# Kernel tuning notes

Measured on AMD Instinct MI355X. Metric: run time of the kernel, lower is better.

The kernel has to match this reference:

```python
import jax, jax.numpy as jnp
import numpy as np

B, PS, E, A, EMB, D, V, LC, TCAP = 128, 14, 2048, 512, 512, 512, 10000, 128, 26
T = TCAP - 1  # max decode length


def setup_inputs() -> dict:
    key = jax.random.key(0)
    ks = jax.random.split(key, 16)
    g = lambda k, shape: jax.random.normal(k, shape, jnp.float32) * 0.02
    cap_len = jax.random.randint(ks[2], (B, 1), 2, TCAP + 1).at[0, 0].set(TCAP)
    return {
        "encoder_out": jax.random.normal(ks[0], (B, PS, PS, E), jnp.float32),
        "encoded_captions": jax.random.randint(ks[1], (B, TCAP), 0, V),
        "caption_lengths": cap_len,
        "length_class": jax.random.randint(ks[3], (B,), 0, 3),
        "W_enc_att": g(ks[4], (E, A)), "b_enc_att": jnp.zeros((A,), jnp.float32),
        "W_dec_att": g(ks[5], (D, A)), "b_dec_att": jnp.zeros((A,), jnp.float32),
        "w_full_att": g(ks[6], (A,)), "b_full_att": jnp.zeros((), jnp.float32),
        "W_init_h": g(ks[7], (E, D)), "b_init_h": jnp.zeros((D,), jnp.float32),
        "W_init_c": g(ks[8], (E, D)), "b_init_c": jnp.zeros((D,), jnp.float32),
        "W_fbeta": g(ks[9], (D, E)), "b_fbeta": jnp.zeros((E,), jnp.float32),
        "emb_table": jax.random.uniform(ks[10], (V, EMB), jnp.float32, -0.1, 0.1),
        "lc_table": jax.random.uniform(ks[11], (3, LC), jnp.float32, -0.1, 0.1),
        "W_fc": jax.random.uniform(ks[12], (D, V), jnp.float32, -0.1, 0.1),
        "b_fc": jnp.zeros((V,), jnp.float32),
        "W_ih": g(ks[13], (EMB + E + LC, 4 * D)), "b_ih": jnp.zeros((4 * D,), jnp.float32),
        "W_hh": g(ks[14], (D, 4 * D)), "b_hh": jnp.zeros((4 * D,), jnp.float32),
    }


def reference(encoder_out, encoded_captions, caption_lengths, length_class,
              W_enc_att, b_enc_att, W_dec_att, b_dec_att, w_full_att, b_full_att,
              W_init_h, b_init_h, W_init_c, b_init_c, W_fbeta, b_fbeta,
              emb_table, lc_table, W_fc, b_fc, W_ih, b_ih, W_hh, b_hh):
    enc = encoder_out.reshape(B, -1, E)                      # [B, P, E]
    cap_len = caption_lengths[:, 0]
    sort_ind = jnp.argsort(-cap_len)                          # descending by length
    enc = enc[sort_ind]
    caps = encoded_captions[sort_ind]
    style = lc_table[length_class[sort_ind]]                  # [B, LC]
    dec_len = cap_len[sort_ind] - 1                           # [B]

    embs = emb_table[caps]                                    # [B, TCAP, EMB]
    mean_enc = enc.mean(axis=1)
    h0 = mean_enc @ W_init_h + b_init_h
    c0 = mean_enc @ W_init_c + b_init_c
    # encoder side of attention is time-invariant: precompute once
    att1 = jnp.einsum('bpe,ea->bpa', enc, W_enc_att) + b_enc_att

    def step(carry, xs):
        h, c = carry
        t, emb_t = xs
        att2 = h @ W_dec_att + b_dec_att
        e = jnp.einsum('bpa,a->bp', jax.nn.relu(att1 + att2[:, None, :]), w_full_att) + b_full_att
        alpha = jax.nn.softmax(e, axis=1)                     # [B, P]
        awe = jnp.einsum('bpe,bp->be', enc, alpha)
        gate = jax.nn.sigmoid(h @ W_fbeta + b_fbeta)
        x = jnp.concatenate([emb_t, style, gate * awe], axis=1)
        gates = x @ W_ih + b_ih + h @ W_hh + b_hh             # [B, 4D], order i,f,g,o
        i, f, g, o = jnp.split(gates, 4, axis=1)
        c_new = jax.nn.sigmoid(f) * c + jax.nn.sigmoid(i) * jnp.tanh(g)
        h_new = jax.nn.sigmoid(o) * jnp.tanh(c_new)
        preds = h_new @ W_fc + b_fc                           # dropout is identity in eval
        m = (t < dec_len)[:, None]                            # active sequences at step t
        return ((jnp.where(m, h_new, h), jnp.where(m, c_new, c)),
                (jnp.where(m, preds, 0.0), jnp.where(m, alpha, 0.0)))

    ts = jnp.arange(T)
    emb_seq = jnp.swapaxes(embs[:, :T, :], 0, 1)              # [T, B, EMB]
    _, (preds, alphas) = jax.lax.scan(step, (h0, c0), (ts, emb_seq))
    predictions = jnp.swapaxes(preds, 0, 1)                   # [B, T, V]
    alphas = jnp.swapaxes(alphas, 0, 1)                       # [B, T, P]
    return predictions, caps, dec_len, alphas, sort_ind
```

## Files before the change

### kernel.cpp

```cpp
#include <hip/hip_runtime.h>
#include <math.h>

constexpr int kB   = 128;
constexpr int kP   = 196;
constexpr int kE   = 2048;
constexpr int kA   = 512;
constexpr int kEMB = 512;
constexpr int kD   = 512;
constexpr int kV   = 10000;
constexpr int kLC  = 128;
constexpr int kTCAP= 26;
constexpr int kT   = 25;
constexpr int kX   = kEMB + kLC + kE;
constexpr int kXH  = kX + kD;
constexpr int kN3  = kV + kA + kE;
constexpr int kBIG = 1 << 30;
constexpr int KZ   = 5;

typedef __attribute__((ext_vector_type(8))) short bf8;
typedef __attribute__((ext_vector_type(4))) float f4;

__device__ inline float b2f(ushort u) { return __uint_as_float(((unsigned)u) << 16); }
__device__ inline ushort f2b(float f) {
    unsigned u = __float_as_uint(f);
    return (ushort)((u + 0x7fffu + ((u >> 16) & 1u)) >> 16);
}

#define SWZ(r, k) ((((r) * 32) + (k)) ^ (((r) & 7) << 3))

__global__ __launch_bounds__(128) void sort_setup(
    const int* __restrict__ caplen, const int* __restrict__ caps_in,
    const int* __restrict__ lclass, const float* __restrict__ lc_table,
    int* __restrict__ sort_ind, int* __restrict__ declen, int* __restrict__ caps_i,
    float* __restrict__ style,
    float* __restrict__ out_caps, float* __restrict__ out_declen,
    float* __restrict__ out_sortind)
{
    __shared__ int lens[kB];
    __shared__ int sind[kB];
    int i = threadIdx.x;
    lens[i] = caplen[i];
    __syncthreads();
    int li = lens[i];
    int r = 0;
    for (int j = 0; j < kB; j++) {
        int lj = lens[j];
        if (lj > li || (lj == li && j < i)) r++;
    }
    sind[r] = i;
    sort_ind[r] = i;
    out_sortind[r] = (float)i;
    __syncthreads();
    int orig = sind[i];
    int dl = lens[orig] - 1;
    declen[i] = dl;
    out_declen[i] = (float)dl;
    for (int t = 0; t < kTCAP; t++) {
        int cv = caps_in[orig * kTCAP + t];
        caps_i[i * kTCAP + t] = cv;
        out_caps[i * kTCAP + t] = (float)cv;
    }
    int lcl = lclass[orig];
    for (int k = 0; k < kLC; k++) style[i * kLC + k] = lc_table[lcl * kLC + k];
}

__global__ __launch_bounds__(256) void tcvt_kernel(
    const float* __restrict__ src, int ldsrc, int K, int N,
    ushort* __restrict__ dst, long long ldd)
{
    __shared__ float tile[32][33];
    int k0 = blockIdx.y * 32, n0 = blockIdx.x * 32;
    int tx = threadIdx.x & 31, ty = threadIdx.x >> 5;
    #pragma unroll
    for (int j = 0; j < 4; j++) {
        int k = k0 + ty + j * 8, n = n0 + tx;
        tile[ty + j * 8][tx] = (k < K && n < N) ? src[(long long)k * ldsrc + n] : 0.f;
    }
    __syncthreads();
    #pragma unroll
    for (int j = 0; j < 4; j++) {
        int n = n0 + ty + j * 8, k = k0 + tx;
        if (n < N && k < K) dst[(long long)n * ldd + k] = f2b(tile[tx][ty + j * 8]);
    }
}

__global__ __launch_bounds__(256) void bias_setup_kernel(
    const float* __restrict__ b_fc, const float* __restrict__ b_dec,
    const float* __restrict__ b_fb, const float* __restrict__ b_ih0,
    const float* __restrict__ b_ic0, const float* __restrict__ b_ih,
    const float* __restrict__ b_hh,
    float* __restrict__ bias3, float* __restrict__ bias_hc, float* __restrict__ gbias)
{
    int idx = blockIdx.x * 256 + threadIdx.x;
    if (idx < kN3) {
        float v;
        if (idx < kV) v = b_fc[idx];
        else if (idx < kV + kA) v = b_dec[idx - kV];
        else v = b_fb[idx - kV - kA];
        bias3[idx] = v;
    } else if (idx < kN3 + 1024) {
        int i = idx - kN3;
        bias_hc[i] = (i < 512) ? b_ih0[i] : b_ic0[i - 512];
    } else if (idx < kN3 + 1024 + 2048) {
        int i = idx - kN3 - 1024;
        gbias[i] = b_ih[i] + b_hh[i];
    }
}

__global__ __launch_bounds__(256) void enc_cvt_kernel(
    const float* __restrict__ enc, const int* __restrict__ sort_ind,
    ushort* __restrict__ enc_bf)
{
    long long idx4 = (long long)blockIdx.x * 256 + threadIdx.x;
    if (idx4 >= (long long)kB * kP * kE / 4) return;
    int r = (int)(idx4 >> 9);
    int cc = ((int)idx4 & 511) * 4;
    int b = r / kP, p = r - b * kP;
    long long srow = (long long)sort_ind[b] * kP + p;
    float4 v = *(const float4*)(enc + srow * kE + cc);
    ushort4 o; o.x = f2b(v.x); o.y = f2b(v.y); o.z = f2b(v.z); o.w = f2b(v.w);
    *(ushort4*)(enc_bf + (long long)r * kE + cc) = o;
}

__global__ __launch_bounds__(256) void mean_enc_kernel(
    const float* __restrict__ encf, const ushort* __restrict__ encb, int use_bf,
    const int* __restrict__ sort_ind, float* __restrict__ me)
{
    int idx = blockIdx.x * 256 + threadIdx.x;
    int b = idx >> 11, e = idx & 2047;
    float s = 0.f;
    if (use_bf) {
        const ushort* base = encb + (long long)b * kP * kE + e;
        #pragma unroll 4
        for (int p = 0; p < kP; p++) s += b2f(base[(long long)p * kE]);
    } else {
        const float* base = encf + (long long)sort_ind[b] * kP * kE + e;
        #pragma unroll 4
        for (int p = 0; p < kP; p++) s += base[(long long)p * kE];
    }
    me[idx] = s * (1.0f / 196.0f);
}

__global__ __launch_bounds__(256) void gemm2(
    const void* __restrict__ Am, int lda, int a_bf16,
    const ushort* __restrict__ Bt, int ldbt,
    const float* __restrict__ bias,
    void* __restrict__ out1, long long ldc1, int c1_bf16,
    int split1, float* __restrict__ out2, long long ldc2,
    int split2, float* __restrict__ out3, long long ldc3,
    const int* __restrict__ declen, int t, int pred_mode,
    int M, int N, int K, long long zstride)
{
    __shared__ short As[64 * 32];
    __shared__ short Bs[128 * 32];
    int tid = threadIdx.x;
    int lane = tid & 63, w = tid >> 6, quad = lane >> 4, l16 = lane & 15;
    int m0 = blockIdx.y * 64, n0 = blockIdx.x * 128;

    f4 acc[8];
    #pragma unroll
    for (int i = 0; i < 8; i++) acc[i] = (f4){0.f, 0.f, 0.f, 0.f};

    int a_r = tid >> 2;
    int a_kc = (tid & 3) * 8;
    long long a_row = m0 + a_r;
    const float*  a_srcf = (const float*)Am  + a_row * (long long)lda + a_kc;
    const ushort* a_srcb = (const ushort*)Am + a_row * (long long)lda + a_kc;

    int b_r = tid >> 1;
    int b_kc = (tid & 1) * 16;
    bool bvalid = (n0 + b_r) < N;
    const ushort* b_src = Bt + (long long)(n0 + b_r) * ldbt + b_kc;

    int kpb = K / (int)gridDim.z;
    int kbeg = (int)blockIdx.z * kpb, kend = kbeg + kpb;

    float4 af0 = make_float4(0.f, 0.f, 0.f, 0.f), af1 = af0;
    uint4 au, bu0, bu1;
    au.x = au.y = au.z = au.w = 0u; bu0 = au; bu1 = au;

    if (a_bf16) au = *(const uint4*)(a_srcb + kbeg);
    else { af0 = *(const float4*)(a_srcf + kbeg); af1 = *(const float4*)(a_srcf + kbeg + 4); }
    if (bvalid) { bu0 = *(const uint4*)(b_src + kbeg); bu1 = *(const uint4*)(b_src + kbeg + 8); }

    for (int k0 = kbeg; k0 < kend; k0 += 32) {
        __syncthreads();
        if (a_bf16) {
            *(uint4*)&As[SWZ(a_r, a_kc)] = au;
        } else {
            uint4 pk; ushort* pp = (ushort*)&pk;
            pp[0] = f2b(af0.x); pp[1] = f2b(af0.y); pp[2] = f2b(af0.z); pp[3] = f2b(af0.w);
            pp[4] = f2b(af1.x); pp[5] = f2b(af1.y); pp[6] = f2b(af1.z); pp[7] = f2b(af1.w);
            *(uint4*)&As[SWZ(a_r, a_kc)] = pk;
        }
        *(uint4*)&Bs[SWZ(b_r, b_kc)]     = bu0;
        *(uint4*)&Bs[SWZ(b_r, b_kc + 8)] = bu1;
        int kn = k0 + 32;
        if (kn < kend) {
            if (a_bf16) au = *(const uint4*)(a_srcb + kn);
            else { af0 = *(const float4*)(a_srcf + kn); af1 = *(const float4*)(a_srcf + kn + 4); }
            if (bvalid) { bu0 = *(const uint4*)(b_src + kn); bu1 = *(const uint4*)(b_src + kn + 8); }
        }
        __syncthreads();
        bf8 a = *(const bf8*)&As[SWZ(w * 16 + l16, quad * 8)];
        #pragma unroll
        for (int nt = 0; nt < 8; nt++) {
            bf8 b = *(const bf8*)&Bs[SWZ(nt * 16 + l16, quad * 8)];
            acc[nt] = __builtin_amdgcn_mfma_f32_16x16x32_bf16(a, b, acc[nt], 0, 0, 0);
        }
    }

    long long zoff = (long long)blockIdx.z * zstride;
    #pragma unroll
    for (int nt = 0; nt < 8; nt++) {
        int cn = n0 + nt * 16 + l16;
        if (cn >= N) continue;
        float bv = bias ? bias[cn] : 0.f;
        #pragma unroll
        for (int reg = 0; reg < 4; reg++) {
            int rr = m0 + w * 16 + quad * 4 + reg;
            float v = acc[nt][reg] + bv;
            if (cn < split1) {
                long long idx;
                if (pred_mode) {
                    int bb = rr & 127, tt = rr >> 7;
                    if (tt >= declen[bb]) v = 0.f;
                    idx = ((long long)bb * kT + tt) * ldc1 + cn;
                } else {
                    if (declen && t >= declen[rr]) v = 0.f;
                    idx = (long long)rr * ldc1 + cn + zoff;
                }
                if (c1_bf16) ((ushort*)out1)[idx] = f2b(v);
                else         ((float*)out1)[idx] = v;
            } else if (cn < split2) {
                out2[(long long)rr * ldc2 + (cn - split1)] = v;
            } else {
                out3[(long long)rr * ldc3 + (cn - split2)] = v;
            }
        }
    }
}

__global__ __launch_bounds__(512) void attn_softmax_kernel(
    const ushort* __restrict__ att1, const float* __restrict__ att2,
    const float* __restrict__ w_full, const float* __restrict__ b_full,
    float* __restrict__ alpha, float* __restrict__ alphas_out,
    const int* __restrict__ declen, int t, const int* __restrict__ smap)
{
    int b = blockIdx.x;
    int ob = smap ? smap[b] : b;
    __shared__ float es[kP];
    __shared__ float red1[8], red2[8];
    int tid = threadIdx.x;
    int wave = tid >> 6, lane = tid & 63;
    float a2r[8], wfr[8];
    {
        const float4* ap = (const float4*)(att2 + (long long)b * kA + lane * 8);
        *(float4*)&a2r[0] = ap[0]; *(float4*)&a2r[4] = ap[1];
        const float4* wp = (const float4*)(w_full + lane * 8);
        *(float4*)&wfr[0] = wp[0]; *(float4*)&wfr[4] = wp[1];
    }
    float bf = b_full[0];
    const ushort* a1base = att1 + (long long)ob * kP * kA + lane * 8;
    for (int p0 = 0; p0 < kP; p0 += 8) {
        int p = p0 + wave;
        if (p < kP) {
            uint4 u = *(const uint4*)(a1base + (long long)p * kA);
            const unsigned* uw = (const unsigned*)&u;
            float s = 0.f;
            #pragma unroll
            for (int j = 0; j < 4; j++) {
                unsigned x = uw[j];
                float v0 = b2f((ushort)(x & 0xffffu)) + a2r[2 * j];
                float v1 = b2f((ushort)(x >> 16))     + a2r[2 * j + 1];
                s += fmaxf(v0, 0.f) * wfr[2 * j] + fmaxf(v1, 0.f) * wfr[2 * j + 1];
            }
            #pragma unroll
            for (int off = 32; off; off >>= 1) s += __shfl_down(s, off);
            if (lane == 0) es[p] = s + bf;
        }
    }
    __syncthreads();
    float e = (tid < kP) ? es[tid] : -1e30f;
    float wm = e;
    for (int off = 32; off; off >>= 1) wm = fmaxf(wm, __shfl_down(wm, off));
    if (lane == 0) red1[wave] = wm;
    __syncthreads();
    float gm = red1[0];
    #pragma unroll
    for (int i = 1; i < 8; i++) gm = fmaxf(gm, red1[i]);
    float ex = (tid < kP) ? expf(e - gm) : 0.f;
    float sw = ex;
    for (int off = 32; off; off >>= 1) sw += __shfl_down(sw, off);
    if (lane == 0) red2[wave] = sw;
    __syncthreads();
    float S = red2[0];
    #pragma unroll
    for (int i = 1; i < 8; i++) S += red2[i];
    if (tid < kP) {
        float a = ex / S;
        alpha[b * kP + tid] = a;
        alphas_out[((long long)b * kT + t) * kP + tid] = (t < declen[b]) ? a : 0.f;
    }
}

__global__ __launch_bounds__(128) void awe_buildx_kernel(
    const float* __restrict__ encf, const ushort* __restrict__ encb, int use_bf,
    const int* __restrict__ sort_ind, const float* __restrict__ alpha,
    const float* __restrict__ gate, const int* __restrict__ caps_i, int t,
    const float* __restrict__ emb_table, const float* __restrict__ style,
    float* __restrict__ xh)
{
    int b = blockIdx.y;
    int tid = threadIdx.x;
    if (blockIdx.x == 4) {
        int tok = caps_i[b * kTCAP + t];
        for (int i = tid; i < 160; i += 128) {
            float4 v;
            if (i < 128) v = *(const float4*)(emb_table + (long long)tok * kEMB + i * 4);
            else         v = *(const float4*)(style + b * kLC + (i - 128) * 4);
            *(float4*)(xh + (long long)b * kXH + i * 4) = v;
        }
        return;
    }
    __shared__ float al[kP];
    for (int i = tid; i < kP; i += 128) al[i] = alpha[b * kP + i];
    __syncthreads();
    int c0 = blockIdx.x * 512 + tid * 4;
    float a0 = 0.f, a1 = 0.f, a2 = 0.f, a3 = 0.f;
    if (use_bf) {
        const ushort* base = encb + (long long)b * kP * kE + c0;
        #pragma unroll 4
        for (int p = 0; p < kP; p++) {
            uint2 u = *(const uint2*)(base + (long long)p * kE);
            float ap = al[p];
            a0 += b2f((ushort)(u.x & 0xffffu)) * ap;
            a1 += b2f((ushort)(u.x >> 16))     * ap;
            a2 += b2f((ushort)(u.y & 0xffffu)) * ap;
            a3 += b2f((ushort)(u.y >> 16))     * ap;
        }
    } else {
        const float* base = encf + (long long)sort_ind[b] * kP * kE + c0;
        #pragma unroll 4
        for (int p = 0; p < kP; p++) {
            float4 v = *(const float4*)(base + (long long)p * kE);
            float ap = al[p];
            a0 += v.x * ap; a1 += v.y * ap; a2 += v.z * ap; a3 += v.w * ap;
        }
    }
    float4 g = *(const float4*)(gate + (long long)b * kE + c0);
    float4 o;
    o.x = a0 / (1.f + expf(-g.x));
    o.y = a1 / (1.f + expf(-g.y));
    o.z = a2 / (1.f + expf(-g.z));
    o.w = a3 / (1.f + expf(-g.w));
    *(float4*)(xh + (long long)b * kXH + kEMB + kLC + c0) = o;
}

__global__ __launch_bounds__(256) void lstm_cell_kernel(
    const float* __restrict__ gpart, const float* __restrict__ gbias,
    float* __restrict__ xh, float* __restrict__ c,
    ushort* __restrict__ Hbuf, int t)
{
    int idx = blockIdx.x * 256 + threadIdx.x;
    int b = idx >> 9, d = idx & 511;
    float gi = gbias[d], gf = gbias[kD + d], gg = gbias[2 * kD + d], go = gbias[3 * kD + d];
    const float* g = gpart + (long long)b * 4 * kD + d;
    #pragma unroll
    for (int z = 0; z < KZ; z++) {
        const float* gz = g + (long long)z * kB * 4 * kD;
        gi += gz[0]; gf += gz[kD]; gg += gz[2 * kD]; go += gz[3 * kD];
    }
    float si = 1.f / (1.f + expf(-gi));
    float sf = 1.f / (1.f + expf(-gf));
    float so = 1.f / (1.f + expf(-go));
    float cn = sf * c[idx] + si * tanhf(gg);
    float hn = so * tanhf(cn);
    c[idx] = cn;
    xh[(long long)b * kXH + kX + d] = hn;
    Hbuf[((long long)t * kB + b) * kD + d] = f2b(hn);
}

extern "C" void kernel_launch(void* const* d_in, const int* in_sizes, int n_in,
                              void* d_out, int out_size, void* d_ws, size_t ws_size,
                              hipStream_t stream)
{
    const float* encoder_out  = (const float*)d_in[0];
    const int*   enc_caps     = (const int*)  d_in[1];
    const int*   cap_lengths  = (const int*)  d_in[2];
    const int*   length_class = (const int*)  d_in[3];
    const float* W_enc_att = (const float*)d_in[4];
    const float* b_enc_att = (const float*)d_in[5];
    const float* W_dec_att = (const float*)d_in[6];
    const float* b_dec_att = (const float*)d_in[7];
    const float* w_full_att = (const float*)d_in[8];
    const float* b_full_att = (const float*)d_in[9];
    const float* W_init_h = (const float*)d_in[10];
    const float* b_init_h = (const float*)d_in[11];
    const float* W_init_c = (const float*)d_in[12];
    const float* b_init_c = (const float*)d_in[13];
    const float* W_fbeta  = (const float*)d_in[14];
    const float* b_fbeta  = (const float*)d_in[15];
    const float* emb_table = (const float*)d_in[16];
    const float* lc_table  = (const float*)d_in[17];
    const float* W_fc = (const float*)d_in[18];
    const float* b_fc = (const float*)d_in[19];
    const float* W_ih = (const float*)d_in[20];
    const float* b_ih = (const float*)d_in[21];
    const float* W_hh = (const float*)d_in[22];
    const float* b_hh = (const float*)d_in[23];

    float* out = (float*)d_out;
    float* o_pred    = out;
    float* o_caps    = out + (long long)kB * kT * kV;
    float* o_declen  = o_caps + kB * kTCAP;
    float* o_alpha   = o_declen + kB;
    float* o_sortind = o_alpha + (long long)kB * kT * kP;

    float* w = (float*)d_ws;
    float* xh       = w; w += kB * kXH;
    float* c        = w; w += kB * kD;
    float* att2     = w; w += kB * kA;
    float* gate     = w; w += kB * kE;
    float* mean_enc = w; w += kB * kE;
    float* gpart    = w; w += (long long)kB * 4 * kD * KZ;
    float* alpha    = w; w += kB * kP;
    float* style    = w; w += kB * kLC;
    float* bias3    = w; w += kN3;
    float* bias_hc  = w; w += 1024;
    float* gbias    = w; w += 2048;
    ushort* us = (ushort*)w;
    ushort* att1_bf  = us; us += (long long)kB * kP * kA;
    ushort* WencT    = us; us += (long long)kA * kE;
    ushort* WhcT     = us; us += (long long)1024 * kE;
    ushort* WcatT    = us; us += (long long)(4 * kD) * kXH;
    ushort* Wcat3T   = us; us += (long long)kN3 * kD;
    ushort* Hbuf     = us; us += (long long)kT * kB * kD;
    int* iw = (int*)us;
    int* sort_ind = iw; iw += kB;
    int* declen   = iw; iw += kB;
    int* caps_i   = iw; iw += kB * kTCAP;
    ushort* enc_bf = (ushort*)(iw + kB);

    size_t need_with_enc = ((char*)(enc_bf + (long long)kB * kP * kE)) - (char*)d_ws;
    int use_encbf = (ws_size >= need_with_enc) ? 1 : 0;

    sort_setup<<<1, 128, 0, stream>>>(cap_lengths, enc_caps, length_class, lc_table,
        sort_ind, declen, caps_i, style, o_caps, o_declen, o_sortind);

    auto tc = [&](const float* s, int ldsrc, int Kr, int Nc, ushort* d, long long ldd) {
        tcvt_kernel<<<dim3((Nc + 31) / 32, (Kr + 31) / 32), 256, 0, stream>>>(
            s, ldsrc, Kr, Nc, d, ldd);
    };
    tc(W_enc_att, kA, kE, kA, WencT, kE);
    tc(W_init_h,  kD, kE, kD, WhcT, kE);
    tc(W_init_c,  kD, kE, kD, WhcT + (long long)kD * kE, kE);
    tc(W_ih, 4 * kD, kX, 4 * kD, WcatT, kXH);
    tc(W_hh, 4 * kD, kD, 4 * kD, WcatT + kX, kXH);
    tc(W_fc,      kV, kD, kV, Wcat3T, kD);
    tc(W_dec_att, kA, kD, kA, Wcat3T + (long long)kV * kD, kD);
    tc(W_fbeta,   kE, kD, kE, Wcat3T + (long long)(kV + kA) * kD, kD);
    bias_setup_kernel<<<(kN3 + 1024 + 2048 + 255) / 256, 256, 0, stream>>>(
        b_fc, b_dec_att, b_fbeta, b_init_h, b_init_c, b_ih, b_hh, bias3, bias_hc, gbias);

    if (use_encbf) {
        enc_cvt_kernel<<<(unsigned)(((long long)kB * kP * kE / 4 + 255) / 256), 256, 0, stream>>>(
            encoder_out, sort_ind, enc_bf);
    }
    mean_enc_kernel<<<(kB * kE) / 256, 256, 0, stream>>>(
        encoder_out, enc_bf, use_encbf, sort_ind, mean_enc);

    auto g2 = [](int M, int N) { return dim3((unsigned)((N + 127) / 128), (unsigned)(M / 64)); };

    gemm2<<<g2(kB, 1024), 256, 0, stream>>>(mean_enc, kE, 0, WhcT, kE, bias_hc,
        xh + kX, kXH, 0, 512, c, kD, kBIG, nullptr, 0, nullptr, 0, 0,
        kB, 1024, kE, 0);

    if (use_encbf) {
        gemm2<<<g2(kB * kP, kA), 256, 0, stream>>>(enc_bf, kE, 1, WencT, kE, b_enc_att,
            att1_bf, kA, 1, kBIG, nullptr, 0, kBIG, nullptr, 0, nullptr, 0, 0,
            kB * kP, kA, kE, 0);
    } else {
        gemm2<<<g2(kB * kP, kA), 256, 0, stream>>>(encoder_out, kE, 0, WencT, kE, b_enc_att,
            att1_bf, kA, 1, kBIG, nullptr, 0, kBIG, nullptr, 0, nullptr, 0, 0,
            kB * kP, kA, kE, 0);
    }

    gemm2<<<g2(kB, kA + kE), 256, 0, stream>>>(xh + kX, kXH, 0,
        Wcat3T + (long long)kV * kD, kD, bias3 + kV, att2, kA, 0,
        kA, gate, kE, kBIG, nullptr, 0, nullptr, 0, 0, kB, kA + kE, kD, 0);

    const int* smap = use_encbf ? nullptr : sort_ind;
    for (int t = 0; t < kT; t++) {
        attn_softmax_kernel<<<kB, 512, 0, stream>>>(att1_bf, att2, w_full_att,
            b_full_att, alpha, o_alpha, declen, t, smap);
        awe_buildx_kernel<<<dim3(5, kB), 128, 0, stream>>>(
            encoder_out, enc_bf, use_encbf, sort_ind, alpha, gate, caps_i, t,
            emb_table, style, xh);
        gemm2<<<dim3((4 * kD + 127) / 128, kB / 64, KZ), 256, 0, stream>>>(
            xh, kXH, 0, WcatT, kXH, nullptr,
            gpart, 4 * kD, 0, kBIG, nullptr, 0, kBIG, nullptr, 0, nullptr, 0, 0,
            kB, 4 * kD, kXH, (long long)kB * 4 * kD);
        lstm_cell_kernel<<<(kB * kD) / 256, 256, 0, stream>>>(gpart, gbias, xh, c, Hbuf, t);
        gemm2<<<g2(kB, kA + kE), 256, 0, stream>>>(xh + kX, kXH, 0,
            Wcat3T + (long long)kV * kD, kD, bias3 + kV, att2, kA, 0,
            kA, gate, kE, kBIG, nullptr, 0, nullptr, 0, 0, kB, kA + kE, kD, 0);
    }

    gemm2<<<g2(kT * kB, kV), 256, 0, stream>>>(Hbuf, kD, 1, Wcat3T, kD, bias3,
        o_pred, kV, 0, kV, nullptr, 0, kBIG, nullptr, 0, declen, 0, 1,
        kT * kB, kV, kD, 0);
}
```

Before: 2.833 ms.

## Fuse attention softmax with AWE build and add 128x128 MFMA GEMM for large matmuls

Merges the per-step attention-softmax and attention-weighted-encoding kernels into one kernel. Each batch row is split across two blocks that both recompute the softmax, which removes the global alpha round trip and one launch per step. Adds a 128x128-tile bf16 MFMA GEMM with XCD-aware block swizzling and register prefetch. It is used for the encoder attention projection and the final vocabulary projection, and in prediction mode it skips MFMA work for inactive (finished) timesteps. The cost is duplicated softmax work in both halves and a larger-tile kernel that may have lower occupancy.

Measured after the change: 2.737 ms. -3.4%, faster.

```diff
diff --git a/kernel.cpp b/kernel.cpp
--- a/kernel.cpp
+++ b/kernel.cpp
@@ -241,18 +241,120 @@
     }
 }
 
-__global__ __launch_bounds__(512) void attn_softmax_kernel(
+__global__ __launch_bounds__(256) void gemm_big(
+    const ushort* __restrict__ A, int lda,
+    const ushort* __restrict__ Bt, int ldbt,
+    const float* __restrict__ bias,
+    void* __restrict__ out1, long long ldc1, int c1_bf16,
+    const int* __restrict__ declen, int pred_mode,
+    int M, int N, int K)
+{
+    __shared__ short As[128 * 32];
+    __shared__ short Bs[128 * 32];
+    unsigned nwg = gridDim.x * gridDim.y;
+    unsigned lin = blockIdx.y * gridDim.x + blockIdx.x;
+    unsigned q = nwg >> 3, rm = nwg & 7;
+    unsigned xcd = lin & 7, loc = lin >> 3;
+    unsigned swz = (xcd < rm ? xcd * (q + 1) : rm * (q + 1) + (xcd - rm) * q) + loc;
+    int bx = (int)(swz % gridDim.x), by = (int)(swz / gridDim.x);
+    int m0 = by * 128, n0 = bx * 128;
+
+    int tid = threadIdx.x;
+    int lane = tid & 63, w = tid >> 6, quad = lane >> 4, l16 = lane & 15;
+    int wr = w >> 1, wc = w & 1;
+
+    f4 acc[4][4];
+    #pragma unroll
+    for (int m = 0; m < 4; m++)
+        #pragma unroll
+        for (int n = 0; n < 4; n++) acc[m][n] = (f4){0.f, 0.f, 0.f, 0.f};
+
+    bool wact = true;
+    if (pred_mode) wact = declen[wr * 64] > (m0 >> 7);
+
+    int s_r = tid >> 1, s_kc = (tid & 1) * 16;
+    const ushort* a_src = A + (long long)(m0 + s_r) * lda + s_kc;
+    bool bval = (n0 + s_r) < N;
+    const ushort* b_src = Bt + (long long)(n0 + s_r) * ldbt + s_kc;
+
+    uint4 au0, au1, bu0, bu1;
+    au0.x = au0.y = au0.z = au0.w = 0u; au1 = au0; bu0 = au0; bu1 = au0;
+    au0 = *(const uint4*)(a_src);
+    au1 = *(const uint4*)(a_src + 8);
+    if (bval) { bu0 = *(const uint4*)(b_src); bu1 = *(const uint4*)(b_src + 8); }
+
+    for (int k0 = 0; k0 < K; k0 += 32) {
+        __syncthreads();
+        *(uint4*)&As[SWZ(s_r, s_kc)]     = au0;
+        *(uint4*)&As[SWZ(s_r, s_kc + 8)] = au1;
+        *(uint4*)&Bs[SWZ(s_r, s_kc)]     = bu0;
+        *(uint4*)&Bs[SWZ(s_r, s_kc + 8)] = bu1;
+        int kn = k0 + 32;
+        if (kn < K) {
+            au0 = *(const uint4*)(a_src + kn);
+            au1 = *(const uint4*)(a_src + kn + 8);
+            if (bval) { bu0 = *(const uint4*)(b_src + kn); bu1 = *(const uint4*)(b_src + kn + 8); }
+        }
+        __syncthreads();
+        if (wact) {
+            bf8 af[4], bfr[4];
+            #pragma unroll
+            for (int m = 0; m < 4; m++)
+                af[m] = *(const bf8*)&As[SWZ(wr * 64 + m * 16 + l16, quad * 8)];
+            #pragma unroll
+            for (int n = 0; n < 4; n++)
+                bfr[n] = *(const bf8*)&Bs[SWZ(wc * 64 + n * 16 + l16, quad * 8)];
+            #pragma unroll
+            for (int m = 0; m < 4; m++)
+                #pragma unroll
+                for (int n = 0; n < 4; n++)
+                    acc[m][n] = __builtin_amdgcn_mfma_f32_16x16x32_bf16(af[m], bfr[n], acc[m][n], 0, 0, 0);
+        }
+    }
+
+    #pragma unroll
+    for (int n = 0; n < 4; n++) {
+        int cn = n0 + wc * 64 + n * 16 + l16;
+        if (cn >= N) continue;
+        float bv = bias ? bias[cn] : 0.f;
+        #pragma unroll
+        for (int m = 0; m < 4; m++) {
+            #pragma unroll
+            for (int reg = 0; reg < 4; reg++) {
+                int rr = m0 + wr * 64 + m * 16 + quad * 4 + reg;
+                float v = acc[m][n][reg] + bv;
+                long long idx;
+                if (pred_mode) {
+                    int bb = rr & 127, tt = rr >> 7;
+                    if (tt >= declen[bb]) v = 0.f;
+                    idx = ((long long)bb * kT + tt) * ldc1 + cn;
+                } else {
+                    idx = (long long)rr * ldc1 + cn;
+                }
+                if (c1_bf16) ((ushort*)out1)[idx] = f2b(v);
+                else         ((float*)out1)[idx] = v;
+            }
+        }
+    }
+}
+
+__global__ __launch_bounds__(512) void attn_awe_kernel(
     const ushort* __restrict__ att1, const float* __restrict__ att2,
     const float* __restrict__ w_full, const float* __restrict__ b_full,
-    float* __restrict__ alpha, float* __restrict__ alphas_out,
-    const int* __restrict__ declen, int t, const int* __restrict__ smap)
-{
-    int b = blockIdx.x;
+    const float* __restrict__ encf, const ushort* __restrict__ encb, int use_bf,
+    const int* __restrict__ sort_ind, const float* __restrict__ gate,
+    const int* __restrict__ caps_i, int t,
+    const float* __restrict__ emb_table, const float* __restrict__ style,
+    float* __restrict__ xh, float* __restrict__ alphas_out,
+    const int* __restrict__ declen, const int* __restrict__ smap)
+{
+    int b = blockIdx.y;
+    int half = blockIdx.x;
     int ob = smap ? smap[b] : b;
-    __shared__ float es[kP];
+    __shared__ float al[kP];
     __shared__ float red1[8], red2[8];
-    int tid = threadIdx.x;
-    int wave = tid >> 6, lane = tid & 63;
+    int tid = threadIdx.x, wave = tid >> 6, lane = tid & 63;
+
     float a2r[8], wfr[8];
     {
         const float4* ap = (const float4*)(att2 + (long long)b * kA + lane * 8);
@@ -260,28 +362,36 @@
         const float4* wp = (const float4*)(w_full + lane * 8);
         *(float4*)&wfr[0] = wp[0]; *(float4*)&wfr[4] = wp[1];
     }
-    float bf = b_full[0];
-    const ushort* a1base = att1 + (long long)ob * kP * kA + lane * 8;
-    for (int p0 = 0; p0 < kP; p0 += 8) {
-        int p = p0 + wave;
-        if (p < kP) {
-            uint4 u = *(const uint4*)(a1base + (long long)p * kA);
-            const unsigned* uw = (const unsigned*)&u;
+    float bfull = b_full[0];
+    const ushort* a1 = att1 + (long long)ob * kP * kA + lane * 8;
+    for (int i0 = 0; i0 < 25; i0 += 4) {
+        uint4 u[4]; int pv[4];
+        #pragma unroll
+        for (int j = 0; j < 4; j++) {
+            int i = i0 + j, p = wave + 8 * i;
+            pv[j] = (i < 25 && p < kP) ? p : -1;
+            if (pv[j] >= 0) u[j] = *(const uint4*)(a1 + (long long)pv[j] * kA);
+        }
+        #pragma unroll
+        for (int j = 0; j < 4; j++) {
+            if (pv[j] < 0) continue;
+            const unsigned* uw = (const unsigned*)&u[j];
             float s = 0.f;
             #pragma unroll
-            for (int j = 0; j < 4; j++) {
-                unsigned x = uw[j];
-                float v0 = b2f((ushort)(x & 0xffffu)) + a2r[2 * j];
-                float v1 = b2f((ushort)(x >> 16))     + a2r[2 * j + 1];
-                s += fmaxf(v0, 0.f) * wfr[2 * j] + fmaxf(v1, 0.f) * wfr[2 * j + 1];
+            for (int q = 0; q < 4; q++) {
+                unsigned x = uw[q];
+                float v0 = b2f((ushort)(x & 0xffffu)) + a2r[2 * q];
+                float v1 = b2f((ushort)(x >> 16))     + a2r[2 * q + 1];
+                s += fmaxf(v0, 0.f) * wfr[2 * q] + fmaxf(v1, 0.f) * wfr[2 * q + 1];
             }
             #pragma unroll
             for (int off = 32; off; off >>= 1) s += __shfl_down(s, off);
-            if (lane == 0) es[p] = s + bf;
-        }
-    }
-    __syncthreads();
-    float e = (tid < kP) ? es[tid] : -1e30f;
+            if (lane == 0) al[pv[j]] = s + bfull;
+        }
+    }
+    __syncthreads();
+
+    float e = (tid < kP) ? al[tid] : -1e30f;
     float wm = e;
     for (int off = 32; off; off >>= 1) wm = fmaxf(wm, __shfl_down(wm, off));
     if (lane == 0) red1[wave] = wm;
@@ -297,64 +407,48 @@
     float S = red2[0];
     #pragma unroll
     for (int i = 1; i < 8; i++) S += red2[i];
+    float a = ex / S;
+    __syncthreads();
     if (tid < kP) {
-        float a = ex / S;
-        alpha[b * kP + tid] = a;
-        alphas_out[((long long)b * kT + t) * kP + tid] = (t < declen[b]) ? a : 0.f;
-    }
-}
-
-__global__ __launch_bounds__(128) void awe_buildx_kernel(
-    const float* __restrict__ encf, const ushort* __restrict__ encb, int use_bf,
-    const int* __restrict__ sort_ind, const float* __restrict__ alpha,
-    const float* __restrict__ gate, const int* __restrict__ caps_i, int t,
-    const float* __restrict__ emb_table, const float* __restrict__ style,
-    float* __restrict__ xh)
-{
-    int b = blockIdx.y;
-    int tid = threadIdx.x;
-    if (blockIdx.x == 4) {
+        al[tid] = a;
+        if (half == 0)
+            alphas_out[((long long)b * kT + t) * kP + tid] = (t < declen[b]) ? a : 0.f;
+    }
+    __syncthreads();
+
+    if (half == 1 && tid < 160) {
         int tok = caps_i[b * kTCAP + t];
-        for (int i = tid; i < 160; i += 128) {
-            float4 v;
-            if (i < 128) v = *(const float4*)(emb_table + (long long)tok * kEMB + i * 4);
-            else         v = *(const float4*)(style + b * kLC + (i - 128) * 4);
-            *(float4*)(xh + (long long)b * kXH + i * 4) = v;
-        }
-        return;
-    }
-    __shared__ float al[kP];
-    for (int i = tid; i < kP; i += 128) al[i] = alpha[b * kP + i];
-    __syncthreads();
-    int c0 = blockIdx.x * 512 + tid * 4;
-    float a0 = 0.f, a1 = 0.f, a2 = 0.f, a3 = 0.f;
+        float4 v;
+        if (tid < 128) v = *(const float4*)(emb_table + (long long)tok * kEMB + tid * 4);
+        else           v = *(const float4*)(style + b * kLC + (tid - 128) * 4);
+        *(float4*)(xh + (long long)b * kXH + tid * 4) = v;
+    }
+
+    int c0 = half * 1024 + tid * 2;
+    float s0 = 0.f, s1 = 0.f;
     if (use_bf) {
         const ushort* base = encb + (long long)b * kP * kE + c0;
         #pragma unroll 4
         for (int p = 0; p < kP; p++) {
-            uint2 u = *(const uint2*)(base + (long long)p * kE);
+            unsigned uu = *(const unsigned*)(base + (long long)p * kE);
             float ap = al[p];
-            a0 += b2f((ushort)(u.x & 0xffffu)) * ap;
-            a1 += b2f((ushort)(u.x >> 16))     * ap;
-            a2 += b2f((ushort)(u.y & 0xffffu)) * ap;
-            a3 += b2f((ushort)(u.y >> 16))     * ap;
+            s0 += b2f((ushort)(uu & 0xffffu)) * ap;
+            s1 += b2f((ushort)(uu >> 16))     * ap;
         }
     } else {
         const float* base = encf + (long long)sort_ind[b] * kP * kE + c0;
         #pragma unroll 4
         for (int p = 0; p < kP; p++) {
-            float4 v = *(const float4*)(base + (long long)p * kE);
+            float2 v = *(const float2*)(base + (long long)p * kE);
             float ap = al[p];
-            a0 += v.x * ap; a1 += v.y * ap; a2 += v.z * ap; a3 += v.w * ap;
-        }
-    }
-    float4 g = *(const float4*)(gate + (long long)b * kE + c0);
-    float4 o;
-    o.x = a0 / (1.f + expf(-g.x));
-    o.y = a1 / (1.f + expf(-g.y));
-    o.z = a2 / (1.f + expf(-g.z));
-    o.w = a3 / (1.f + expf(-g.w));
-    *(float4*)(xh + (long long)b * kXH + kEMB + kLC + c0) = o;
+            s0 += v.x * ap; s1 += v.y * ap;
+        }
+    }
+    float2 g = *(const float2*)(gate + (long long)b * kE + c0);
+    float2 o;
+    o.x = s0 / (1.f + expf(-g.x));
+    o.y = s1 / (1.f + expf(-g.y));
+    *(float2*)(xh + (long long)b * kXH + kEMB + kLC + c0) = o;
 }
 
 __global__ __launch_bounds__(256) void lstm_cell_kernel(
@@ -424,7 +518,6 @@
     float* gate     = w; w += kB * kE;
     float* mean_enc = w; w += kB * kE;
     float* gpart    = w; w += (long long)kB * 4 * kD * KZ;
-    float* alpha    = w; w += kB * kP;
     float* style    = w; w += kB * kLC;
     float* bias3    = w; w += kN3;
     float* bias_hc  = w; w += 1024;
@@ -477,9 +570,9 @@
         kB, 1024, kE, 0);
 
     if (use_encbf) {
-        gemm2<<<g2(kB * kP, kA), 256, 0, stream>>>(enc_bf, kE, 1, WencT, kE, b_enc_att,
-            att1_bf, kA, 1, kBIG, nullptr, 0, kBIG, nullptr, 0, nullptr, 0, 0,
-            kB * kP, kA, kE, 0);
+        gemm_big<<<dim3(kA / 128, kB * kP / 128), 256, 0, stream>>>(
+            enc_bf, kE, WencT, kE, b_enc_att,
+            att1_bf, kA, 1, nullptr, 0, kB * kP, kA, kE);
     } else {
         gemm2<<<g2(kB * kP, kA), 256, 0, stream>>>(encoder_out, kE, 0, WencT, kE, b_enc_att,
             att1_bf, kA, 1, kBIG, nullptr, 0, kBIG, nullptr, 0, nullptr, 0, 0,
@@ -492,11 +585,9 @@
 
     const int* smap = use_encbf ? nullptr : sort_ind;
     for (int t = 0; t < kT; t++) {
-        attn_softmax_kernel<<<kB, 512, 0, stream>>>(att1_bf, att2, w_full_att,
-            b_full_att, alpha, o_alpha, declen, t, smap);
-        awe_buildx_kernel<<<dim3(5, kB), 128, 0, stream>>>(
-            encoder_out, enc_bf, use_encbf, sort_ind, alpha, gate, caps_i, t,
-            emb_table, style, xh);
+        attn_awe_kernel<<<dim3(2, kB), 512, 0, stream>>>(att1_bf, att2, w_full_att,
+            b_full_att, encoder_out, enc_bf, use_encbf, sort_ind, gate, caps_i, t,
+            emb_table, style, xh, o_alpha, declen, smap);
         gemm2<<<dim3((4 * kD + 127) / 128, kB / 64, KZ), 256, 0, stream>>>(
             xh, kXH, 0, WcatT, kXH, nullptr,
             gpart, 4 * kD, 0, kBIG, nullptr, 0, kBIG, nullptr, 0, nullptr, 0, 0,
@@ -507,7 +598,7 @@
             kA, gate, kE, kBIG, nullptr, 0, nullptr, 0, 0, kB, kA + kE, kD, 0);
     }
 
-    gemm2<<<g2(kT * kB, kV), 256, 0, stream>>>(Hbuf, kD, 1, Wcat3T, kD, bias3,
-        o_pred, kV, 0, kV, nullptr, 0, kBIG, nullptr, 0, declen, 0, 1,
-        kT * kB, kV, kD, 0);
-}
+    gemm_big<<<dim3((kV + 127) / 128, kT * kB / 128), 256, 0, stream>>>(
+        Hbuf, kD, Wcat3T, kD, bias3,
+        o_pred, kV, 0, declen, 1, kT * kB, kV, kD);
+}
```
